# Kernel optimization log

Measured on AMD Instinct MI355X. Metric: run time of the kernel, lower is better.

## Reference

```python
import jax, jax.numpy as jnp
import numpy as np

B, S, D = 4, 4096, 1024
H, HKV, DH = 16, 4, 64
C = 256            # chunk_size
HALF_W = 128       # sliding_window // 2 (attend iff |i-j| <= HALF_W)
EPS = 1e-6


def _rope_tables(seq_len, dh):
    inv_freq = 1.0 / (10000.0 ** (np.arange(0, dh, 2, dtype=np.float32) / dh))
    t = np.arange(seq_len, dtype=np.float32)
    ang = np.einsum('s,f->sf', t, inv_freq)          # [S, dh/2]
    emb = np.concatenate([ang, ang], axis=-1)        # [S, dh]
    return jnp.asarray(np.cos(emb)), jnp.asarray(np.sin(emb))


def setup_inputs() -> dict:
    key = jax.random.key(0)
    ks = jax.random.split(key, 6)
    w = 0.02
    cos, sin = _rope_tables(S, DH)
    return {
        'x':  jax.random.normal(ks[0], (B, S, D), dtype=jnp.float32),
        'Wq': jax.random.normal(ks[1], (D, H * DH), dtype=jnp.float32) * w,
        'bq': jnp.zeros((H * DH,), jnp.float32),
        'Wk': jax.random.normal(ks[2], (D, HKV * DH), dtype=jnp.float32) * w,
        'bk': jnp.zeros((HKV * DH,), jnp.float32),
        'Wv': jax.random.normal(ks[3], (D, HKV * DH), dtype=jnp.float32) * w,
        'bv': jnp.zeros((HKV * DH,), jnp.float32),
        'Wo': jax.random.normal(ks[4], (H * DH, D), dtype=jnp.float32) * w,
        'bo': jnp.zeros((D,), jnp.float32),
        'qn_w': jnp.ones((DH,), jnp.float32),
        'kn_w': jnp.ones((DH,), jnp.float32),
        'cos': cos,
        'sin': sin,
    }


def _rmsnorm(t, w):
    var = jnp.mean(t * t, axis=-1, keepdims=True)
    return t * jax.lax.rsqrt(var + EPS) * w


def _rotate_half(t):
    t1, t2 = jnp.split(t, 2, axis=-1)
    return jnp.concatenate([-t2, t1], axis=-1)


def _apply_rope(t, cos, sin):
    # t: [B, h, S, dh]; cos/sin: [S, dh]
    return t * cos[None, None] + _rotate_half(t) * sin[None, None]


def _neighbor_blocks(t, nc):
    # t: [B, h, S, dh] -> [B, h, nc, 3C, dh] (prev, cur, next chunk; zero-padded ends)
    tp = jnp.pad(t, ((0, 0), (0, 0), (C, C), (0, 0)))
    tp = tp.reshape(t.shape[0], t.shape[1], nc + 2, C, t.shape[-1])
    return jnp.concatenate([tp[:, :, :-2], tp[:, :, 1:-1], tp[:, :, 2:]], axis=3)


def forward(x, Wq, bq, Wk, bk, Wv, bv, Wo, bo, qn_w, kn_w, cos, sin):
    b, s, _ = x.shape
    nc = s // C
    q = (x @ Wq + bq).reshape(b, s, H, DH).transpose(0, 2, 1, 3)     # [B,H,S,dh]
    k = (x @ Wk + bk).reshape(b, s, HKV, DH).transpose(0, 2, 1, 3)   # [B,Hkv,S,dh]
    v = (x @ Wv + bv).reshape(b, s, HKV, DH).transpose(0, 2, 1, 3)
    q = _rmsnorm(q, qn_w)
    k = _rmsnorm(k, kn_w)
    q = _apply_rope(q, cos, sin)
    k = _apply_rope(k, cos, sin)
    # GQA: repeat kv heads
    rep = H // HKV
    k = jnp.repeat(k, rep, axis=1)
    v = jnp.repeat(v, rep, axis=1)

    qc = q.reshape(b, H, nc, C, DH)
    kb = _neighbor_blocks(k, nc)   # [B,H,nc,3C,dh]
    vb = _neighbor_blocks(v, nc)

    scale = 1.0 / np.sqrt(DH).astype(np.float32)
    scores = jnp.einsum('bhncd,bhnkd->bhnck', qc, kb) * scale        # [B,H,nc,C,3C]

    iq = jnp.arange(C)[:, None]                  # query pos within chunk
    jk = jnp.arange(3 * C)[None, :]              # key pos within block
    rel = jk - C - iq                            # key_global - query_global
    c_idx = jnp.arange(nc)[:, None, None]
    gkj = (c_idx - 1) * C + jk[None]             # global key index [nc,C,3C]
    mask = (jnp.abs(rel)[None] <= HALF_W) & (gkj >= 0) & (gkj < s)
    scores = jnp.where(mask[None, None], scores, jnp.float32(-1e30))
    attn = jax.nn.softmax(scores, axis=-1)
    out = jnp.einsum('bhnck,bhnkd->bhncd', attn, vb)                 # [B,H,nc,C,dh]
    out = out.reshape(b, H, s, DH).transpose(0, 2, 1, 3).reshape(b, s, H * DH)
    return out @ Wo + bo


def reference(x, Wq, bq, Wk, bk, Wv, bv, Wo, bo, qn_w, kn_w, cos, sin):
    return forward(x, Wq, bq, Wk, bk, Wv, bv, Wo, bo, qn_w, kn_w, cos, sin)
```

## Files before the change

kernel.cpp:

```cpp
#include <hip/hip_runtime.h>
#include <stdint.h>

typedef __bf16 bf16_t;
typedef __bf16 bf16x8 __attribute__((ext_vector_type(8)));
typedef __bf16 bf16x4 __attribute__((ext_vector_type(4)));
typedef float  f32x4  __attribute__((ext_vector_type(4)));

#define MFMA_BF16(a,b,c) __builtin_amdgcn_mfma_f32_16x16x32_bf16((a),(b),(c),0,0,0)

constexpr int kB = 4;
constexpr int kS = 4096;
constexpr int kD = 1024;
constexpr int kH = 16;
constexpr int kHKV = 4;
constexpr int kDH = 64;
constexpr int kChunk = 256;

__device__ __forceinline__ void gload_lds16(const bf16_t* g, bf16_t* l){
  __builtin_amdgcn_global_load_lds((const __attribute__((address_space(1))) void*)g,
                                   (__attribute__((address_space(3))) void*)l, 16, 0, 0);
}

__device__ __forceinline__ void lds_fence(){
  asm volatile("s_waitcnt lgkmcnt(0)" ::: "memory");
  __builtin_amdgcn_sched_barrier(0);
}

__global__ __launch_bounds__(256) void k_cvt_bf16(const float* __restrict__ in,
                                                  bf16_t* __restrict__ out, int n4){
  int i = blockIdx.x * 256 + threadIdx.x;
  if (i >= n4) return;
  float4 v = ((const float4*)in)[i];
  bf16x4 o;
  o[0] = (__bf16)v.x; o[1] = (__bf16)v.y; o[2] = (__bf16)v.z; o[3] = (__bf16)v.w;
  ((bf16x4*)out)[i] = o;
}

__global__ __launch_bounds__(256) void k_transpose_cvt(const float* __restrict__ W,
                                                       bf16_t* __restrict__ Wt,
                                                       int K, int N){
  __shared__ float t[32][33];
  int n0 = blockIdx.x * 32, k0 = blockIdx.y * 32;
  int tx = threadIdx.x & 31, ty = threadIdx.x >> 5;
#pragma unroll
  for (int i = 0; i < 4; i++){
    int kkk = ty + i*8;
    t[kkk][tx] = W[(size_t)(k0+kkk)*N + n0 + tx];
  }
  __syncthreads();
#pragma unroll
  for (int i = 0; i < 4; i++){
    int nn = ty + i*8;
    Wt[(size_t)(n0+nn)*K + k0 + tx] = (__bf16)t[tx][nn];
  }
}

template<bool BF16OUT>
__global__ __launch_bounds__(256) void k_gemm_bt(const bf16_t* __restrict__ A,
                                                 const bf16_t* __restrict__ Bt,
                                                 const float* __restrict__ bias,
                                                 void* __restrict__ outp,
                                                 int M, int N, int K){
  (void)M;
  __shared__ bf16_t Al[128*64];
  __shared__ bf16_t Bl[128*64];
  const int tid = threadIdx.x;
  const int lane = tid & 63;
  const int wave = tid >> 6;
  const int wm = wave >> 1, wn = wave & 1;
  const int bm = blockIdx.y, bn = blockIdx.x;
  const int l15 = lane & 15, l4 = lane >> 4;
  const int s_row = lane >> 3;
  const int s_bc  = lane & 7;
  const int s_colE = (s_bc ^ s_row) * 8;
  f32x4 acc[4][4];
#pragma unroll
  for (int a = 0; a < 4; a++)
#pragma unroll
    for (int b = 0; b < 4; b++)
#pragma unroll
      for (int r = 0; r < 4; r++) acc[a][b][r] = 0.f;

  for (int kt = 0; kt < K; kt += 64){
    __syncthreads();
#pragma unroll
    for (int i = 0; i < 4; i++){
      int rowA = (wave*4 + i)*8 + s_row;
      gload_lds16(A  + (size_t)(bm*128 + rowA)*K + kt + s_colE, &Al[(wave*4 + i)*512]);
      gload_lds16(Bt + (size_t)(bn*128 + rowA)*K + kt + s_colE, &Bl[(wave*4 + i)*512]);
    }
    __syncthreads();
#pragma unroll
    for (int ks = 0; ks < 2; ks++){
      bf16x8 af[4], bfr[4];
#pragma unroll
      for (int mt = 0; mt < 4; mt++){
        int row = wm*64 + mt*16 + l15;
        af[mt] = *(const bf16x8*)&Al[(row*64 + ks*32 + l4*8) ^ ((row & 7)*8)];
      }
#pragma unroll
      for (int nt = 0; nt < 4; nt++){
        int row = wn*64 + nt*16 + l15;
        bfr[nt] = *(const bf16x8*)&Bl[(row*64 + ks*32 + l4*8) ^ ((row & 7)*8)];
      }
#pragma unroll
      for (int mt = 0; mt < 4; mt++)
#pragma unroll
        for (int nt = 0; nt < 4; nt++)
          acc[mt][nt] = MFMA_BF16(af[mt], bfr[nt], acc[mt][nt]);
    }
  }
#pragma unroll
  for (int mt = 0; mt < 4; mt++){
#pragma unroll
    for (int nt = 0; nt < 4; nt++){
      int row0 = bm*128 + wm*64 + mt*16 + l4*4;
      int col  = bn*128 + wn*64 + nt*16 + l15;
      float bv = bias[col];
#pragma unroll
      for (int r = 0; r < 4; r++){
        float v = acc[mt][nt][r] + bv;
        if (BF16OUT) ((bf16_t*)outp)[(size_t)(row0 + r)*N + col] = (__bf16)v;
        else         ((float*)outp)[(size_t)(row0 + r)*N + col] = v;
      }
    }
  }
}

__global__ __launch_bounds__(256) void k_norm_rope(const float* __restrict__ qin,
                                                   const float* __restrict__ kin,
                                                   const float* __restrict__ qw,
                                                   const float* __restrict__ kw,
                                                   const float* __restrict__ cosb,
                                                   const float* __restrict__ sinb,
                                                   bf16_t* __restrict__ qout,
                                                   bf16_t* __restrict__ kout){
  const int g = blockIdx.x * 16 + (threadIdx.x >> 4);
  const int ln = threadIdx.x & 15;
  const int NQ = (kB*kS) * kH;
  const float* src; bf16_t* dst; const float* w;
  int row;
  if (g < NQ){
    row = g >> 4; int head = g & 15;
    src = qin + (size_t)row*1024 + head*64;
    dst = qout + (size_t)row*1024 + head*64;
    w = qw;
  } else {
    int gk = g - NQ;
    row = gk >> 2; int head = gk & 3;
    src = kin + (size_t)row*256 + head*64;
    dst = kout + (size_t)row*256 + head*64;
    w = kw;
  }
  float t0 = src[ln], t1 = src[ln+16], t2 = src[ln+32], t3 = src[ln+48];
  float ss = t0*t0 + t1*t1 + t2*t2 + t3*t3;
  ss += __shfl_xor(ss, 1); ss += __shfl_xor(ss, 2);
  ss += __shfl_xor(ss, 4); ss += __shfl_xor(ss, 8);
  float rs = rsqrtf(ss * (1.0f/64.0f) + 1e-6f);
  t0 *= rs * w[ln];    t1 *= rs * w[ln+16];
  t2 *= rs * w[ln+32]; t3 *= rs * w[ln+48];
  int s = row & (kS - 1);
  const float* cp = cosb + (size_t)s*64;
  const float* sp = sinb + (size_t)s*64;
  float o0 = t0*cp[ln]    - t2*sp[ln];
  float o1 = t1*cp[ln+16] - t3*sp[ln+16];
  float o2 = t2*cp[ln+32] + t0*sp[ln+32];
  float o3 = t3*cp[ln+48] + t1*sp[ln+48];
  dst[ln]    = (__bf16)o0; dst[ln+16] = (__bf16)o1;
  dst[ln+32] = (__bf16)o2; dst[ln+48] = (__bf16)o3;
}

__global__ __launch_bounds__(256) void k_attn(const bf16_t* __restrict__ q,
                                              const bf16_t* __restrict__ kbuf,
                                              const bf16_t* __restrict__ vbuf,
                                              bf16_t* __restrict__ o){
  __shared__ bf16_t Vt[4][64][72];
  __shared__ bf16_t Pm[4][16][72];
  const int c = blockIdx.x, h = blockIdx.y, b = blockIdx.z;
  const int hkv = h >> 2;
  const int tid = threadIdx.x;
  const int lane = tid & 63, w = tid >> 6;
  const int l15 = lane & 15, l4 = lane >> 4;
  const int qrow0 = c*kChunk + w*64;

  bf16x8 qf[4][2];
#pragma unroll
  for (int mt = 0; mt < 4; mt++)
#pragma unroll
    for (int ks = 0; ks < 2; ks++)
      qf[mt][ks] = *(const bf16x8*)(q + (size_t)(b*kS + qrow0 + mt*16 + l15)*1024
                                      + h*64 + ks*32 + l4*8);

  f32x4 acc[4][4];
  float m_run[4][4], l_run[4][4];
#pragma unroll
  for (int mt = 0; mt < 4; mt++){
#pragma unroll
    for (int dt = 0; dt < 4; dt++)
#pragma unroll
      for (int r = 0; r < 4; r++) acc[mt][dt][r] = 0.f;
#pragma unroll
    for (int r = 0; r < 4; r++){ m_run[mt][r] = -1e30f; l_run[mt][r] = 0.f; }
  }

  for (int kt = w; kt <= w + 4; kt++){
    const int kg0 = c*kChunk - 128 + kt*64;

    {
      int kg = kg0 + lane;
      bool ok = (kg >= 0) && (kg < kS);
      const bf16_t* vr = vbuf + (size_t)(b*kS + (ok ? kg : 0))*256 + hkv*64;
#pragma unroll
      for (int c8 = 0; c8 < 8; c8++){
        bf16x8 vv8;
        if (ok) vv8 = *(const bf16x8*)(vr + c8*8);
        else {
#pragma unroll
          for (int e = 0; e < 8; e++) vv8[e] = (__bf16)0.f;
        }
#pragma unroll
        for (int e = 0; e < 8; e++) Vt[w][c8*8 + e][lane] = vv8[e];
      }
    }

    bf16x8 kf[4][2];
#pragma unroll
    for (int nt = 0; nt < 4; nt++){
      int kg = kg0 + nt*16 + l15;
      if (kg >= 0 && kg < kS){
        const bf16_t* kr = kbuf + (size_t)(b*kS + kg)*256 + hkv*64;
#pragma unroll
        for (int ks = 0; ks < 2; ks++)
          kf[nt][ks] = *(const bf16x8*)(kr + ks*32 + l4*8);
      } else {
#pragma unroll
        for (int ks = 0; ks < 2; ks++)
#pragma unroll
          for (int e = 0; e < 8; e++) kf[nt][ks][e] = (__bf16)0.f;
      }
    }

#pragma unroll
    for (int mt = 0; mt < 4; mt++){
      f32x4 sc[4];
#pragma unroll
      for (int nt = 0; nt < 4; nt++)
#pragma unroll
        for (int r = 0; r < 4; r++) sc[nt][r] = 0.f;
#pragma unroll
      for (int ks = 0; ks < 2; ks++)
#pragma unroll
        for (int nt = 0; nt < 4; nt++)
          sc[nt] = MFMA_BF16(qf[mt][ks], kf[nt][ks], sc[nt]);

      const int qg0 = qrow0 + mt*16 + l4*4;
#pragma unroll
      for (int nt = 0; nt < 4; nt++){
        int kg = kg0 + nt*16 + l15;
        bool kgok = (kg >= 0) && (kg < kS);
#pragma unroll
        for (int r = 0; r < 4; r++){
          int rel = kg - (qg0 + r);
          bool okm = kgok && (rel >= -128) && (rel <= 128);
          sc[nt][r] = okm ? sc[nt][r]*0.125f : -1e30f;
        }
      }
      float mx[4], fct[4], rsum[4];
#pragma unroll
      for (int r = 0; r < 4; r++){
        mx[r] = fmaxf(fmaxf(sc[0][r], sc[1][r]), fmaxf(sc[2][r], sc[3][r]));
        mx[r] = fmaxf(mx[r], __shfl_xor(mx[r], 1));
        mx[r] = fmaxf(mx[r], __shfl_xor(mx[r], 2));
        mx[r] = fmaxf(mx[r], __shfl_xor(mx[r], 4));
        mx[r] = fmaxf(mx[r], __shfl_xor(mx[r], 8));
        float mn = fmaxf(m_run[mt][r], mx[r]);
        fct[r] = __expf(m_run[mt][r] - mn);
        m_run[mt][r] = mn;
        rsum[r] = 0.f;
      }
#pragma unroll
      for (int nt = 0; nt < 4; nt++)
#pragma unroll
        for (int r = 0; r < 4; r++){
          float p = __expf(sc[nt][r] - m_run[mt][r]);
          rsum[r] += p;
          sc[nt][r] = p;
        }
#pragma unroll
      for (int r = 0; r < 4; r++){
        rsum[r] += __shfl_xor(rsum[r], 1);
        rsum[r] += __shfl_xor(rsum[r], 2);
        rsum[r] += __shfl_xor(rsum[r], 4);
        rsum[r] += __shfl_xor(rsum[r], 8);
        l_run[mt][r] = l_run[mt][r]*fct[r] + rsum[r];
      }
#pragma unroll
      for (int dt = 0; dt < 4; dt++)
#pragma unroll
        for (int r = 0; r < 4; r++) acc[mt][dt][r] *= fct[r];

#pragma unroll
      for (int nt = 0; nt < 4; nt++)
#pragma unroll
        for (int r = 0; r < 4; r++)
          Pm[w][l4*4 + r][nt*16 + l15] = (__bf16)sc[nt][r];

      lds_fence();

      bf16x8 pf0 = *(const bf16x8*)&Pm[w][l15][l4*8];
      bf16x8 pf1 = *(const bf16x8*)&Pm[w][l15][32 + l4*8];
#pragma unroll
      for (int dt = 0; dt < 4; dt++){
        bf16x8 vf0 = *(const bf16x8*)&Vt[w][dt*16 + l15][l4*8];
        bf16x8 vf1 = *(const bf16x8*)&Vt[w][dt*16 + l15][32 + l4*8];
        acc[mt][dt] = MFMA_BF16(pf0, vf0, acc[mt][dt]);
        acc[mt][dt] = MFMA_BF16(pf1, vf1, acc[mt][dt]);
      }
      lds_fence();
    }
  }

#pragma unroll
  for (int mt = 0; mt < 4; mt++)
#pragma unroll
    for (int dt = 0; dt < 4; dt++){
      int row = b*kS + qrow0 + mt*16 + l4*4;
      int col = h*64 + dt*16 + l15;
#pragma unroll
      for (int r = 0; r < 4; r++){
        float ov = acc[mt][dt][r] / l_run[mt][r];
        o[(size_t)(row + r)*1024 + col] = (__bf16)ov;
      }
    }
}

extern "C" void kernel_launch(void* const* d_in, const int* in_sizes, int n_in,
                              void* d_out, int out_size, void* d_ws, size_t ws_size,
                              hipStream_t stream){
  (void)in_sizes; (void)n_in; (void)out_size; (void)ws_size;
  const float* x    = (const float*)d_in[0];
  const float* Wq   = (const float*)d_in[1];
  const float* bq   = (const float*)d_in[2];
  const float* Wk   = (const float*)d_in[3];
  const float* bk   = (const float*)d_in[4];
  const float* Wv   = (const float*)d_in[5];
  const float* bv   = (const float*)d_in[6];
  const float* Wo   = (const float*)d_in[7];
  const float* bo   = (const float*)d_in[8];
  const float* qn_w = (const float*)d_in[9];
  const float* kn_w = (const float*)d_in[10];
  const float* cosb = (const float*)d_in[11];
  const float* sinb = (const float*)d_in[12];
  float* out = (float*)d_out;

  char* ws = (char*)d_ws;
  const size_t MB = 1024ull*1024ull;
  bf16_t* x_b  = (bf16_t*)(ws);
  bf16_t* q_b  = (bf16_t*)(ws + 32*MB);
  bf16_t* k_b  = (bf16_t*)(ws + 64*MB);
  bf16_t* v_b  = (bf16_t*)(ws + 72*MB);
  float*  k_f  = (float*) (ws + 80*MB);
  bf16_t* wq_t = (bf16_t*)(ws + 96*MB);
  bf16_t* wo_t = (bf16_t*)(ws + 98*MB);
  bf16_t* wk_t = (bf16_t*)(ws + 100*MB);
  bf16_t* wv_t = (bf16_t*)(ws + 100*MB + 512*1024);
  bf16_t* attn_b = x_b;
  float*  q_f  = out;

  k_cvt_bf16<<<dim3(16384), dim3(256), 0, stream>>>(x, x_b, (kB*kS*kD)/4);
  k_transpose_cvt<<<dim3(32, 32), dim3(256), 0, stream>>>(Wq, wq_t, 1024, 1024);
  k_transpose_cvt<<<dim3(8, 32),  dim3(256), 0, stream>>>(Wk, wk_t, 1024, 256);
  k_transpose_cvt<<<dim3(8, 32),  dim3(256), 0, stream>>>(Wv, wv_t, 1024, 256);
  k_transpose_cvt<<<dim3(32, 32), dim3(256), 0, stream>>>(Wo, wo_t, 1024, 1024);

  k_gemm_bt<false><<<dim3(8, 128), dim3(256), 0, stream>>>(x_b, wq_t, bq, (void*)q_f, 16384, 1024, 1024);
  k_gemm_bt<false><<<dim3(2, 128), dim3(256), 0, stream>>>(x_b, wk_t, bk, (void*)k_f, 16384, 256, 1024);
  k_gemm_bt<true ><<<dim3(2, 128), dim3(256), 0, stream>>>(x_b, wv_t, bv, (void*)v_b, 16384, 256, 1024);

  k_norm_rope<<<dim3(20480), dim3(256), 0, stream>>>(q_f, k_f, qn_w, kn_w, cosb, sinb, q_b, k_b);

  k_attn<<<dim3(16, 16, 4), dim3(256), 0, stream>>>(q_b, k_b, v_b, attn_b);

  k_gemm_bt<false><<<dim3(8, 128), dim3(256), 0, stream>>>(attn_b, wo_t, bo, (void*)out, 16384, 1024, 1024);
}
```

Measured before the change: 465.4 us.

## Pre-transpose V and split attention into single-wave blocks loading fragments directly

Adds a kernel that transposes V into a [b, hkv*64, S] layout, so the attention kernel can load V MFMA fragments straight from global memory instead of scattering them through LDS. The attention kernel becomes one 64-thread wave per block, with four times as many blocks. Key tiles that fall entirely outside the sequence are skipped, which removes the per-element bounds checks. This drops the LDS V staging and its scalar scatter stores, at the cost of an extra transpose pass over V and more, smaller blocks.

```diff
diff --git a/kernel.cpp b/kernel.cpp
--- a/kernel.cpp
+++ b/kernel.cpp
@@ -52,6 +52,24 @@
   for (int i = 0; i < 4; i++){
     int nn = ty + i*8;
     Wt[(size_t)(n0+nn)*K + k0 + tx] = (__bf16)t[tx][nn];
+  }
+}
+
+__global__ __launch_bounds__(256) void k_transpose_v(const bf16_t* __restrict__ V,
+                                                     bf16_t* __restrict__ vT){
+  __shared__ bf16_t t[32][36];
+  int r0 = blockIdx.x * 32;
+  int c0 = blockIdx.y * 32;
+  int tx = threadIdx.x & 31, ty = threadIdx.x >> 5;
+  int b  = r0 >> 12, s0 = r0 & 4095;
+#pragma unroll
+  for (int i = 0; i < 4; i++)
+    t[ty + i*8][tx] = V[(size_t)(r0 + ty + i*8)*256 + c0 + tx];
+  __syncthreads();
+#pragma unroll
+  for (int i = 0; i < 4; i++){
+    int cc = ty + i*8;
+    vT[(size_t)(b*256 + c0 + cc)*4096 + s0 + tx] = t[tx][cc];
   }
 }
 
@@ -170,18 +188,17 @@
   dst[ln+32] = (__bf16)o2; dst[ln+48] = (__bf16)o3;
 }
 
-__global__ __launch_bounds__(256) void k_attn(const bf16_t* __restrict__ q,
-                                              const bf16_t* __restrict__ kbuf,
-                                              const bf16_t* __restrict__ vbuf,
-                                              bf16_t* __restrict__ o){
-  __shared__ bf16_t Vt[4][64][72];
-  __shared__ bf16_t Pm[4][16][72];
-  const int c = blockIdx.x, h = blockIdx.y, b = blockIdx.z;
+__global__ __launch_bounds__(64, 3) void k_attn2(const bf16_t* __restrict__ q,
+                                                 const bf16_t* __restrict__ kbuf,
+                                                 const bf16_t* __restrict__ vT,
+                                                 bf16_t* __restrict__ o){
+  __shared__ bf16_t Pm[16][72];
+  const int strip = blockIdx.x, h = blockIdx.y, b = blockIdx.z;
+  const int c = strip >> 2, w = strip & 3;
   const int hkv = h >> 2;
-  const int tid = threadIdx.x;
-  const int lane = tid & 63, w = tid >> 6;
+  const int lane = threadIdx.x;
   const int l15 = lane & 15, l4 = lane >> 4;
-  const int qrow0 = c*kChunk + w*64;
+  const int qrow0 = strip*64;
 
   bf16x8 qf[4][2];
 #pragma unroll
@@ -205,39 +222,23 @@
 
   for (int kt = w; kt <= w + 4; kt++){
     const int kg0 = c*kChunk - 128 + kt*64;
-
-    {
-      int kg = kg0 + lane;
-      bool ok = (kg >= 0) && (kg < kS);
-      const bf16_t* vr = vbuf + (size_t)(b*kS + (ok ? kg : 0))*256 + hkv*64;
-#pragma unroll
-      for (int c8 = 0; c8 < 8; c8++){
-        bf16x8 vv8;
-        if (ok) vv8 = *(const bf16x8*)(vr + c8*8);
-        else {
-#pragma unroll
-          for (int e = 0; e < 8; e++) vv8[e] = (__bf16)0.f;
-        }
-#pragma unroll
-        for (int e = 0; e < 8; e++) Vt[w][c8*8 + e][lane] = vv8[e];
-      }
-    }
+    if (kg0 < 0 || kg0 >= kS) continue;
 
     bf16x8 kf[4][2];
 #pragma unroll
     for (int nt = 0; nt < 4; nt++){
-      int kg = kg0 + nt*16 + l15;
-      if (kg >= 0 && kg < kS){
-        const bf16_t* kr = kbuf + (size_t)(b*kS + kg)*256 + hkv*64;
-#pragma unroll
-        for (int ks = 0; ks < 2; ks++)
-          kf[nt][ks] = *(const bf16x8*)(kr + ks*32 + l4*8);
-      } else {
-#pragma unroll
-        for (int ks = 0; ks < 2; ks++)
-#pragma unroll
-          for (int e = 0; e < 8; e++) kf[nt][ks][e] = (__bf16)0.f;
-      }
+      const bf16_t* kr = kbuf + (size_t)(b*kS + kg0 + nt*16 + l15)*256 + hkv*64;
+#pragma unroll
+      for (int ks = 0; ks < 2; ks++)
+        kf[nt][ks] = *(const bf16x8*)(kr + ks*32 + l4*8);
+    }
+    bf16x8 vf[2][4];
+#pragma unroll
+    for (int dt = 0; dt < 4; dt++){
+      const bf16_t* vr = vT + (size_t)(b*256 + hkv*64 + dt*16 + l15)*4096 + kg0;
+#pragma unroll
+      for (int ks = 0; ks < 2; ks++)
+        vf[ks][dt] = *(const bf16x8*)(vr + ks*32 + l4*8);
     }
 
 #pragma unroll
@@ -257,11 +258,10 @@
 #pragma unroll
       for (int nt = 0; nt < 4; nt++){
         int kg = kg0 + nt*16 + l15;
-        bool kgok = (kg >= 0) && (kg < kS);
 #pragma unroll
         for (int r = 0; r < 4; r++){
           int rel = kg - (qg0 + r);
-          bool okm = kgok && (rel >= -128) && (rel <= 128);
+          bool okm = (rel >= -128) && (rel <= 128);
           sc[nt][r] = okm ? sc[nt][r]*0.125f : -1e30f;
         }
       }
@@ -303,18 +303,16 @@
       for (int nt = 0; nt < 4; nt++)
 #pragma unroll
         for (int r = 0; r < 4; r++)
-          Pm[w][l4*4 + r][nt*16 + l15] = (__bf16)sc[nt][r];
+          Pm[l4*4 + r][nt*16 + l15] = (__bf16)sc[nt][r];
 
       lds_fence();
 
-      bf16x8 pf0 = *(const bf16x8*)&Pm[w][l15][l4*8];
-      bf16x8 pf1 = *(const bf16x8*)&Pm[w][l15][32 + l4*8];
+      bf16x8 pf0 = *(const bf16x8*)&Pm[l15][l4*8];
+      bf16x8 pf1 = *(const bf16x8*)&Pm[l15][32 + l4*8];
 #pragma unroll
       for (int dt = 0; dt < 4; dt++){
-        bf16x8 vf0 = *(const bf16x8*)&Vt[w][dt*16 + l15][l4*8];
-        bf16x8 vf1 = *(const bf16x8*)&Vt[w][dt*16 + l15][32 + l4*8];
-        acc[mt][dt] = MFMA_BF16(pf0, vf0, acc[mt][dt]);
-        acc[mt][dt] = MFMA_BF16(pf1, vf1, acc[mt][dt]);
+        acc[mt][dt] = MFMA_BF16(pf0, vf[0][dt], acc[mt][dt]);
+        acc[mt][dt] = MFMA_BF16(pf1, vf[1][dt], acc[mt][dt]);
       }
       lds_fence();
     }
@@ -364,6 +362,7 @@
   bf16_t* wo_t = (bf16_t*)(ws + 98*MB);
   bf16_t* wk_t = (bf16_t*)(ws + 100*MB);
   bf16_t* wv_t = (bf16_t*)(ws + 100*MB + 512*1024);
+  bf16_t* vT_b = (bf16_t*)(ws + 101*MB);
   bf16_t* attn_b = x_b;
   float*  q_f  = out;
 
@@ -378,8 +377,9 @@
   k_gemm_bt<true ><<<dim3(2, 128), dim3(256), 0, stream>>>(x_b, wv_t, bv, (void*)v_b, 16384, 256, 1024);
 
   k_norm_rope<<<dim3(20480), dim3(256), 0, stream>>>(q_f, k_f, qn_w, kn_w, cosb, sinb, q_b, k_b);
-
-  k_attn<<<dim3(16, 16, 4), dim3(256), 0, stream>>>(q_b, k_b, v_b, attn_b);
+  k_transpose_v<<<dim3(512, 8), dim3(256), 0, stream>>>(v_b, vT_b);
+
+  k_attn2<<<dim3(64, 16, 4), dim3(64), 0, stream>>>(q_b, k_b, vT_b, attn_b);
 
   k_gemm_bt<false><<<dim3(8, 128), dim3(256), 0, stream>>>(attn_b, wo_t, bo, (void*)out, 16384, 1024, 1024);
 }
```

Measured after the change: 514.4 us. +10.5%, slower.
